# Kernel tuning notes

Hardware: AMD Instinct MI355X
Metric: run time of the kernel (lower is better)

Reference implementation:

```python
import jax, jax.numpy as jnp
import numpy as np
from jax import lax

WIN = 9
PAD = WIN // 2
DIM = 3
WIN_VOL = WIN ** DIM  # 729
EPS_DENOM = 1e-05


def _box_sum(x):
    # x: (N, 1, D, H, W); all-ones WINxWINxWIN box filter, 'same' padding
    kernel = jnp.ones((1, 1, WIN, WIN, WIN), dtype=x.dtype)
    return lax.conv_general_dilated(
        x, kernel,
        window_strides=(1, 1, 1),
        padding=[(PAD, PAD)] * 3,
        dimension_numbers=("NCDHW", "OIDHW", "NCDHW"),
    )


def setup_inputs() -> dict:
    key = jax.random.key(0)
    k1, k2 = jax.random.split(key)
    shape = (2, 1, 160, 192, 160)
    I = jax.random.uniform(k1, shape, dtype=jnp.float32)
    J = jax.random.uniform(k2, shape, dtype=jnp.float32)
    return {"I": I, "J": J}


def reference(I, J):
    n = I.shape[0]
    # Fuse the five box-filter convs into one by stacking along the batch dim
    stacked = jnp.concatenate([I, J, I * I, J * J, I * J], axis=0)
    sums = _box_sum(stacked)
    I_sum, J_sum, I2_sum, J2_sum, IJ_sum = (
        sums[0 * n:1 * n], sums[1 * n:2 * n], sums[2 * n:3 * n],
        sums[3 * n:4 * n], sums[4 * n:5 * n],
    )
    wv = jnp.asarray(WIN_VOL, dtype=I.dtype)
    E_I = I_sum / wv
    E_J = J_sum / wv
    cross = IJ_sum - I_sum * E_J - J_sum * E_I + E_I * E_J * wv
    I_var = I2_sum - 2 * E_I * I_sum + E_I * E_I * wv
    J_var = J2_sum - 2 * E_J * J_sum + E_J * E_J * wv
    cc = cross * cross / (I_var * J_var + EPS_DENOM)
    return -jnp.mean(cc)
```

## Files before the change

kernel.cpp:

```cpp
#include <hip/hip_runtime.h>


namespace {
constexpr int Wd = 160, Hd = 192, Dd = 160, NB = 2;
constexpr long DSTRIDE = (long)Hd * Wd;
constexpr long VOLUME  = (long)Dd * DSTRIDE;
constexpr long TOTAL   = VOLUME * NB;
constexpr int BW = 32, BH = 16, BD = 28;
constexpr int EH = BH + 8;
constexpr int NWB = 5, NHB = 12, NDB = 6;
constexpr int NBLK = NB * NDB * NHB * NWB;
constexpr int NT = 512;
constexpr int CH = EH * BW;
constexpr float INV_WV = 1.0f / 729.0f;
}

__global__ __launch_bounds__(NT, 4) void k_ncc(const float* __restrict__ I,
                                               const float* __restrict__ J,
                                               float* __restrict__ partial) {
    __shared__ float ws[2][5 * CH];
    __shared__ float red[NT];

    const int tid = threadIdx.x;
    int bx = blockIdx.x;
    const int wb = bx % NWB; bx /= NWB;
    const int hb = bx % NHB; bx /= NHB;
    const int db = bx % NDB; bx /= NDB;
    const int n  = bx;
    const int w0 = wb * BW, h0 = hb * BH, d0 = db * BD;
    const long nvol = (long)n * VOLUME;

    const int seg = tid & 7;
    const int yy  = tid >> 3;
    const int ah  = h0 - 4 + yy;
    const int wbase = w0 - 4 + (seg << 2);
    const bool aJob = (tid < 192);
    const bool ahOk = aJob && ((unsigned)ah < (unsigned)Hd);
    bool qok[3];
#pragma unroll
    for (int q = 0; q < 3; ++q)
        qok[q] = ((unsigned)(wbase + 4 * q) < (unsigned)Wd);
    float* const wa = &ws[0][yy * BW + (seg << 2)];

    const int tx = tid & 31, ty = tid >> 5;
    const float* const rb = &ws[0][ty * BW + tx];

    float hist[9][5];
#pragma unroll
    for (int k = 0; k < 9; ++k)
#pragma unroll
        for (int c = 0; c < 5; ++c) hist[k][c] = 0.0f;
    float sa[5] = {0, 0, 0, 0, 0};
    float acc = 0.0f;

    for (int M = 0; M < 4; ++M) {
#pragma unroll
        for (int u = 0; u < 9; ++u) {
            const int t = 9 * M + u;
            const int p = d0 - 4 + t;
            const bool pvalid = ((unsigned)p < (unsigned)Dd);
            const int bufo = (t & 1) * (5 * CH);

            if (pvalid && aJob) {
                float vi[12], vj[12];
                if (ahOk) {
                    const float* rowI = I + nvol + (long)p * DSTRIDE + (long)ah * Wd;
                    const float* rowJ = J + nvol + (long)p * DSTRIDE + (long)ah * Wd;
#pragma unroll
                    for (int q = 0; q < 3; ++q) {
                        float4 a = qok[q] ? *(const float4*)(rowI + wbase + 4 * q)
                                          : float4{0, 0, 0, 0};
                        float4 b = qok[q] ? *(const float4*)(rowJ + wbase + 4 * q)
                                          : float4{0, 0, 0, 0};
                        vi[4 * q + 0] = a.x; vi[4 * q + 1] = a.y;
                        vi[4 * q + 2] = a.z; vi[4 * q + 3] = a.w;
                        vj[4 * q + 0] = b.x; vj[4 * q + 1] = b.y;
                        vj[4 * q + 2] = b.z; vj[4 * q + 3] = b.w;
                    }
                } else {
#pragma unroll
                    for (int i = 0; i < 12; ++i) { vi[i] = 0.0f; vj[i] = 0.0f; }
                }
                float* const wab = wa + bufo;
#pragma unroll
                for (int c = 0; c < 5; ++c) {
                    float v[12];
#pragma unroll
                    for (int i = 0; i < 12; ++i) {
                        v[i] = (c == 0) ? vi[i]
                             : (c == 1) ? vj[i]
                             : (c == 2) ? vi[i] * vi[i]
                             : (c == 3) ? vj[i] * vj[i]
                                        : vi[i] * vj[i];
                    }
                    float s8 = v[0] + v[1] + v[2] + v[3] + v[4] + v[5] + v[6] + v[7] + v[8];
                    float4 o;
                    o.x = s8;
                    o.y = o.x + (v[9]  - v[0]);
                    o.z = o.y + (v[10] - v[1]);
                    o.w = o.z + (v[11] - v[2]);
                    *(float4*)(wab + c * CH) = o;
                }
            }
            __syncthreads();

            float h5[5];
            if (pvalid) {
                const float* const rbb = rb + bufo;
#pragma unroll
                for (int c = 0; c < 5; ++c) {
                    float tsum = 0.0f;
#pragma unroll
                    for (int dy = 0; dy < 9; ++dy)
                        tsum += rbb[c * CH + dy * BW];
                    h5[c] = tsum;
                }
            } else {
#pragma unroll
                for (int c = 0; c < 5; ++c) h5[c] = 0.0f;
            }
#pragma unroll
            for (int c = 0; c < 5; ++c) sa[c] += h5[c];
            const int dout = d0 + t - 8;
            if (t >= 8 && dout < Dd) {
                const float cross = sa[4] - sa[0] * sa[1] * INV_WV;
                const float iv    = sa[2] - sa[0] * sa[0] * INV_WV;
                const float jv    = sa[3] - sa[1] * sa[1] * INV_WV;
                acc += (cross * cross) / (iv * jv + 1e-5f);
            }
#pragma unroll
            for (int c = 0; c < 5; ++c) sa[c] -= hist[(u + 1) % 9][c];
#pragma unroll
            for (int c = 0; c < 5; ++c) hist[u][c] = h5[c];
        }
    }

    red[tid] = acc;
    __syncthreads();
    for (int off = NT / 2; off > 0; off >>= 1) {
        if (tid < off) red[tid] += red[tid + off];
        __syncthreads();
    }
    if (tid == 0) partial[blockIdx.x] = red[0];
}

__global__ __launch_bounds__(256) void k_final(const float* __restrict__ partial,
                                               float* __restrict__ out, int nparts) {
    __shared__ double red[256];
    double a = 0.0;
    for (int i = threadIdx.x; i < nparts; i += 256) a += (double)partial[i];
    red[threadIdx.x] = a;
    __syncthreads();
    for (int off = 128; off > 0; off >>= 1) {
        if (threadIdx.x < off) red[threadIdx.x] += red[threadIdx.x + off];
        __syncthreads();
    }
    if (threadIdx.x == 0) out[0] = (float)(-red[0] / (double)TOTAL);
}

extern "C" void kernel_launch(void* const* d_in, const int* in_sizes, int n_in,
                              void* d_out, int out_size, void* d_ws, size_t ws_size,
                              hipStream_t stream) {
    const float* I = (const float*)d_in[0];
    const float* J = (const float*)d_in[1];
    float* partial = (float*)d_ws;
    float* out = (float*)d_out;

    k_ncc<<<NBLK, NT, 0, stream>>>(I, J, partial);
    k_final<<<1, 256, 0, stream>>>(partial, out, NBLK);
}
```

Baseline: 185.6 us.

## Prefetch next depth slice, add running H-sum pass in LDS, use fast reciprocal

The global loads for the next depth plane are issued into registers before the barrier, so memory latency overlaps the LDS passes. The 9-tap H-direction sum per thread is replaced by a separate running-sum pass: 320 threads compute sliding sums into a new LDS array, and each thread then reads 5 values instead of 45. The division becomes a hardware reciprocal, and the barriers become a custom waitcnt+s_barrier. In exchange this adds an extra barrier per slice, more LDS, and prefetch registers, and it drops the occupancy hint from launch bounds, which may change register allocation and occupancy.

```diff
diff --git a/kernel.cpp b/kernel.cpp
--- a/kernel.cpp
+++ b/kernel.cpp
@@ -11,14 +11,20 @@
 constexpr int NWB = 5, NHB = 12, NDB = 6;
 constexpr int NBLK = NB * NDB * NHB * NWB;
 constexpr int NT = 512;
-constexpr int CH = EH * BW;
+constexpr int CH  = EH * BW;
+constexpr int HWC = BH * BW;
 constexpr float INV_WV = 1.0f / 729.0f;
 }
 
-__global__ __launch_bounds__(NT, 4) void k_ncc(const float* __restrict__ I,
-                                               const float* __restrict__ J,
-                                               float* __restrict__ partial) {
+__device__ __forceinline__ void bar_lds() {
+    asm volatile("s_waitcnt lgkmcnt(0)\n\ts_barrier" ::: "memory");
+}
+
+__global__ __launch_bounds__(NT) void k_ncc(const float* __restrict__ I,
+                                            const float* __restrict__ J,
+                                            float* __restrict__ partial) {
     __shared__ float ws[2][5 * CH];
+    __shared__ float hw[5 * HWC];
     __shared__ float red[NT];
 
     const int tid = threadIdx.x;
@@ -32,18 +38,43 @@
 
     const int seg = tid & 7;
     const int yy  = tid >> 3;
-    const int ah  = h0 - 4 + yy;
+    const bool aJob = (tid < 192);
+    const int ah    = h0 - 4 + yy;
     const int wbase = w0 - 4 + (seg << 2);
-    const bool aJob = (tid < 192);
     const bool ahOk = aJob && ((unsigned)ah < (unsigned)Hd);
     bool qok[3];
 #pragma unroll
     for (int q = 0; q < 3; ++q)
         qok[q] = ((unsigned)(wbase + 4 * q) < (unsigned)Wd);
-    float* const wa = &ws[0][yy * BW + (seg << 2)];
+    const long roff = nvol + (long)ah * Wd + wbase + (long)(d0 - 4) * DSTRIDE;
+    const float* aI = I + roff;
+    const float* aJ = J + roff;
+
+    const int c2 = tid >> 6;
+    const int h2 = (tid >> 5) & 1;
+    const int w2 = tid & 31;
+    const int ho0 = h2 * 8;
 
     const int tx = tid & 31, ty = tid >> 5;
-    const float* const rb = &ws[0][ty * BW + tx];
+
+    float vi[12], vj[12];
+    auto issue = [&](int p) {
+        const bool pv = ((unsigned)p < (unsigned)Dd);
+        if (aJob) {
+            if (pv && ahOk) {
+#pragma unroll
+                for (int q = 0; q < 3; ++q) {
+                    float4 a = qok[q] ? *(const float4*)(aI + 4 * q) : float4{0, 0, 0, 0};
+                    float4 b = qok[q] ? *(const float4*)(aJ + 4 * q) : float4{0, 0, 0, 0};
+                    vi[4 * q] = a.x; vi[4 * q + 1] = a.y; vi[4 * q + 2] = a.z; vi[4 * q + 3] = a.w;
+                    vj[4 * q] = b.x; vj[4 * q + 1] = b.y; vj[4 * q + 2] = b.z; vj[4 * q + 3] = b.w;
+                }
+            } else {
+#pragma unroll
+                for (int i = 0; i < 12; ++i) { vi[i] = 0.0f; vj[i] = 0.0f; }
+            }
+        }
+    };
 
     float hist[9][5];
 #pragma unroll
@@ -53,35 +84,19 @@
     float sa[5] = {0, 0, 0, 0, 0};
     float acc = 0.0f;
 
+    issue(d0 - 4);
+
+#pragma unroll 1
     for (int M = 0; M < 4; ++M) {
 #pragma unroll
         for (int u = 0; u < 9; ++u) {
             const int t = 9 * M + u;
             const int p = d0 - 4 + t;
             const bool pvalid = ((unsigned)p < (unsigned)Dd);
-            const int bufo = (t & 1) * (5 * CH);
+            float* const wsp = ws[t & 1];
 
             if (pvalid && aJob) {
-                float vi[12], vj[12];
-                if (ahOk) {
-                    const float* rowI = I + nvol + (long)p * DSTRIDE + (long)ah * Wd;
-                    const float* rowJ = J + nvol + (long)p * DSTRIDE + (long)ah * Wd;
-#pragma unroll
-                    for (int q = 0; q < 3; ++q) {
-                        float4 a = qok[q] ? *(const float4*)(rowI + wbase + 4 * q)
-                                          : float4{0, 0, 0, 0};
-                        float4 b = qok[q] ? *(const float4*)(rowJ + wbase + 4 * q)
-                                          : float4{0, 0, 0, 0};
-                        vi[4 * q + 0] = a.x; vi[4 * q + 1] = a.y;
-                        vi[4 * q + 2] = a.z; vi[4 * q + 3] = a.w;
-                        vj[4 * q + 0] = b.x; vj[4 * q + 1] = b.y;
-                        vj[4 * q + 2] = b.z; vj[4 * q + 3] = b.w;
-                    }
-                } else {
-#pragma unroll
-                    for (int i = 0; i < 12; ++i) { vi[i] = 0.0f; vj[i] = 0.0f; }
-                }
-                float* const wab = wa + bufo;
+                float* const wab = wsp + yy * BW + (seg << 2);
 #pragma unroll
                 for (int c = 0; c < 5; ++c) {
                     float v[12];
@@ -93,7 +108,8 @@
                              : (c == 3) ? vj[i] * vj[i]
                                         : vi[i] * vj[i];
                     }
-                    float s8 = v[0] + v[1] + v[2] + v[3] + v[4] + v[5] + v[6] + v[7] + v[8];
+                    float s8 = ((v[0] + v[1]) + (v[2] + v[3]))
+                             + ((v[4] + v[5]) + (v[6] + v[7])) + v[8];
                     float4 o;
                     o.x = s8;
                     o.y = o.x + (v[9]  - v[0]);
@@ -102,19 +118,31 @@
                     *(float4*)(wab + c * CH) = o;
                 }
             }
-            __syncthreads();
+            aI += DSTRIDE; aJ += DSTRIDE;
+            issue(p + 1);
+
+            bar_lds();
+
+            if (pvalid && tid < 320) {
+                const float* const src = wsp + c2 * CH + ho0 * BW + w2;
+                float* const dst = hw + c2 * HWC + ho0 * BW + w2;
+                float s = ((src[0 * BW] + src[1 * BW]) + (src[2 * BW] + src[3 * BW]))
+                        + ((src[4 * BW] + src[5 * BW]) + (src[6 * BW] + src[7 * BW]));
+#pragma unroll
+                for (int k = 0; k < 8; ++k) {
+                    s += src[(k + 8) * BW];
+                    dst[k * BW] = s;
+                    s -= src[k * BW];
+                }
+            }
+
+            bar_lds();
 
             float h5[5];
             if (pvalid) {
-                const float* const rbb = rb + bufo;
 #pragma unroll
-                for (int c = 0; c < 5; ++c) {
-                    float tsum = 0.0f;
-#pragma unroll
-                    for (int dy = 0; dy < 9; ++dy)
-                        tsum += rbb[c * CH + dy * BW];
-                    h5[c] = tsum;
-                }
+                for (int c = 0; c < 5; ++c)
+                    h5[c] = hw[c * HWC + ty * BW + tx];
             } else {
 #pragma unroll
                 for (int c = 0; c < 5; ++c) h5[c] = 0.0f;
@@ -126,7 +154,7 @@
                 const float cross = sa[4] - sa[0] * sa[1] * INV_WV;
                 const float iv    = sa[2] - sa[0] * sa[0] * INV_WV;
                 const float jv    = sa[3] - sa[1] * sa[1] * INV_WV;
-                acc += (cross * cross) / (iv * jv + 1e-5f);
+                acc += (cross * cross) * __builtin_amdgcn_rcpf(iv * jv + 1e-5f);
             }
 #pragma unroll
             for (int c = 0; c < 5; ++c) sa[c] -= hist[(u + 1) % 9][c];
```

After: 209.8 us. 1.13x slower.
